# Kernel tuning notes

Measured on AMD Instinct MI355X. Metric: run time of the kernel, lower is better.

The kernel has to match this reference:

```python
import jax, jax.numpy as jnp
import numpy as np

HIDDEN_DIM = 2048
CODE_DIM = 256
CODEBOOK_SIZE = 512
FC_DIMS = [1024, 512]
BATCH = 16384
EPS = 1e-5
NEG_SLOPE = 0.01  # PyTorch LeakyReLU default


def _linear_init(key, fan_in, fan_out):
    # kaiming_uniform_(a=sqrt(3)) ~= U(-1/sqrt(fan_in), 1/sqrt(fan_in)) scaled; use uniform bound
    bound = 1.0 / np.sqrt(fan_in)
    return jax.random.uniform(key, (fan_in, fan_out), jnp.float32, -bound, bound)


def setup_inputs() -> dict:
    key = jax.random.key(0)
    ks = jax.random.split(key, 16)
    h = jax.random.normal(ks[0], (BATCH, HIDDEN_DIM), jnp.float32)
    # encoder: Linear(2048->1024, no bias), BN, LReLU, Linear(1024->512, no bias), BN, LReLU, Linear(512->256, bias)
    enc_w1 = _linear_init(ks[1], HIDDEN_DIM, FC_DIMS[0])
    enc_bn1_g = jnp.ones((FC_DIMS[0],), jnp.float32)
    enc_bn1_b = jnp.zeros((FC_DIMS[0],), jnp.float32)
    enc_w2 = _linear_init(ks[2], FC_DIMS[0], FC_DIMS[1])
    enc_bn2_g = jnp.ones((FC_DIMS[1],), jnp.float32)
    enc_bn2_b = jnp.zeros((FC_DIMS[1],), jnp.float32)
    enc_w3 = _linear_init(ks[3], FC_DIMS[1], CODE_DIM)
    enc_b3 = jax.random.uniform(ks[4], (CODE_DIM,), jnp.float32, -1/np.sqrt(FC_DIMS[1]), 1/np.sqrt(FC_DIMS[1]))
    # codebook: NearestEmbed weight shape (code_dim, codebook_size)
    codebook = jax.random.normal(ks[5], (CODE_DIM, CODEBOOK_SIZE), jnp.float32)
    # decoder: Linear(256->512, no bias), BN, LReLU, Linear(512->1024, no bias), BN, LReLU, Linear(1024->2048, bias)
    dec_w1 = _linear_init(ks[6], CODE_DIM, FC_DIMS[1])
    dec_bn1_g = jnp.ones((FC_DIMS[1],), jnp.float32)
    dec_bn1_b = jnp.zeros((FC_DIMS[1],), jnp.float32)
    dec_w2 = _linear_init(ks[7], FC_DIMS[1], FC_DIMS[0])
    dec_bn2_g = jnp.ones((FC_DIMS[0],), jnp.float32)
    dec_bn2_b = jnp.zeros((FC_DIMS[0],), jnp.float32)
    dec_w3 = _linear_init(ks[8], FC_DIMS[0], HIDDEN_DIM)
    dec_b3 = jax.random.uniform(ks[9], (HIDDEN_DIM,), jnp.float32, -1/np.sqrt(FC_DIMS[0]), 1/np.sqrt(FC_DIMS[0]))
    return dict(h=h, enc_w1=enc_w1, enc_bn1_g=enc_bn1_g, enc_bn1_b=enc_bn1_b,
                enc_w2=enc_w2, enc_bn2_g=enc_bn2_g, enc_bn2_b=enc_bn2_b,
                enc_w3=enc_w3, enc_b3=enc_b3, codebook=codebook,
                dec_w1=dec_w1, dec_bn1_g=dec_bn1_g, dec_bn1_b=dec_bn1_b,
                dec_w2=dec_w2, dec_bn2_g=dec_bn2_g, dec_bn2_b=dec_bn2_b,
                dec_w3=dec_w3, dec_b3=dec_b3)


def _bn(x, g, b):
    # BatchNorm1d, training mode: biased batch variance, eps=1e-5
    mu = jnp.mean(x, axis=0)
    var = jnp.var(x, axis=0)
    return (x - mu) * jax.lax.rsqrt(var + EPS) * g + b


def _lrelu(x):
    return jnp.where(x >= 0, x, NEG_SLOPE * x)


def _quantize(z_e, codebook):
    # nearest codebook entry; codebook is [code_dim, K]
    # dist[b,k] = ||z_e[b] - codebook[:,k]||^2 (expanded, drop constant ||z||^2 for argmin? keep full for clarity)
    d = (jnp.sum(z_e * z_e, axis=1, keepdims=True)
         - 2.0 * (z_e @ codebook)
         + jnp.sum(codebook * codebook, axis=0)[None, :])  # [B, K]
    idx = jnp.argmin(d, axis=1)  # [B]
    z_q = codebook.T[idx]        # [B, code_dim]
    return z_q, idx


def reference(h, enc_w1, enc_bn1_g, enc_bn1_b, enc_w2, enc_bn2_g, enc_bn2_b,
              enc_w3, enc_b3, codebook,
              dec_w1, dec_bn1_g, dec_bn1_b, dec_w2, dec_bn2_g, dec_bn2_b,
              dec_w3, dec_b3):
    # encoder
    x = _lrelu(_bn(h @ enc_w1, enc_bn1_g, enc_bn1_b))
    x = _lrelu(_bn(x @ enc_w2, enc_bn2_g, enc_bn2_b))
    z_e = x @ enc_w3 + enc_b3  # [B, code_dim]
    # nearest-embed quantization with straight-through estimator
    z_q_raw, code_indices = _quantize(z_e, codebook)
    z_q = z_e + jax.lax.stop_gradient(z_q_raw - z_e)
    # decoder
    y = _lrelu(_bn(z_q @ dec_w1, dec_bn1_g, dec_bn1_b))
    y = _lrelu(_bn(y @ dec_w2, dec_bn2_g, dec_bn2_b))
    h_recon = y @ dec_w3 + dec_b3  # [B, hidden_dim]
    return z_e, z_q, h_recon, code_indices
```

## Files before the change

kernel.cpp:

```cpp
#include <hip/hip_runtime.h>
#include <hip/hip_fp16.h>
#include <cstdint>
#include <cstddef>

typedef _Float16 f16;
typedef _Float16 half8 __attribute__((ext_vector_type(8)));
typedef _Float16 half4 __attribute__((ext_vector_type(4)));
typedef float floatx4 __attribute__((ext_vector_type(4)));

static constexpr size_t NB  = 16384;
static constexpr size_t DH  = 2048;
static constexpr size_t F1  = 1024;
static constexpr size_t F2  = 512;
static constexpr size_t CD  = 256;
static constexpr size_t KCB = 512;

static constexpr size_t ZE_OFF  = 0;
static constexpr size_t ZQ_OFF  = NB * CD;
static constexpr size_t HR_OFF  = 2 * NB * CD;
static constexpr size_t IDX_OFF = 2 * NB * CD + NB * DH;

static constexpr size_t O_HH   = 0;
static constexpr size_t O_HL   = O_HH + NB * DH * 2;
static constexpr size_t R1_END = O_HL + NB * DH * 2;

static constexpr size_t R_X1H = 0;
static constexpr size_t R_X1L = NB * F1 * 2;
static constexpr size_t R_X2F = 2 * NB * F1 * 2;
static constexpr size_t R_X2H = R_X2F + NB * F2 * 4;
static constexpr size_t R_X2L = R_X2H + NB * F2 * 2;
static constexpr size_t R_Y1F = 0;
static constexpr size_t R_Y1H = NB * F2 * 4;
static constexpr size_t R_Y2H = 0;

static constexpr size_t O_W1H = R1_END;
static constexpr size_t O_W1L = O_W1H + F1 * DH * 2;
static constexpr size_t O_W2H = O_W1L + F1 * DH * 2;
static constexpr size_t O_W2L = O_W2H + F2 * F1 * 2;
static constexpr size_t O_W3H = O_W2L + F2 * F1 * 2;
static constexpr size_t O_W3L = O_W3H + CD * F2 * 2;
static constexpr size_t O_CBH = O_W3L + CD * F2 * 2;
static constexpr size_t O_CBL = O_CBH + KCB * CD * 2;
static constexpr size_t O_DW1 = O_CBL + KCB * CD * 2;
static constexpr size_t O_DW2 = O_DW1 + F2 * CD * 2;
static constexpr size_t O_DW3 = O_DW2 + F1 * F2 * 2;
static constexpr size_t O_SUM = O_DW3 + DH * F1 * 2;
static constexpr size_t O_SQ  = O_SUM + 4 * 1024 * 8;
static constexpr size_t O_SC  = O_SQ + 4 * 1024 * 8;
static constexpr size_t O_SH  = O_SC + 4 * 1024 * 4;
static constexpr size_t O_CN  = O_SH + 4 * 1024 * 4;
static constexpr size_t R2    = (O_CN + 4096 + 255) & ~(size_t)255;
static constexpr size_t R2_X1F = R2;
static constexpr size_t R2_ZEH = R2;
static constexpr size_t R2_ZEL = R2 + NB * CD * 2;
static constexpr size_t R2_S   = R2 + 2 * NB * CD * 2;
static constexpr size_t R2_ZQH = R2_S + NB * KCB * 4;
static constexpr size_t R2_Y2F = R2;

#define GLLDS(src, dst)                                                          \
    __builtin_amdgcn_global_load_lds(                                            \
        (const __attribute__((address_space(1))) void*)(src),                    \
        (__attribute__((address_space(3))) void*)(dst), 16, 0, 0)

#define VMCNT(n)  asm volatile("s_waitcnt vmcnt(" #n ")" ::: "memory")
#define LGKMCNT0  asm volatile("s_waitcnt lgkmcnt(0)" ::: "memory")

#define WAITC(n) do { switch (n) {                                               \
    case 0: asm volatile("s_waitcnt lgkmcnt(0)" ::: "memory"); break;            \
    case 1: asm volatile("s_waitcnt lgkmcnt(1)" ::: "memory"); break;            \
    case 2: asm volatile("s_waitcnt lgkmcnt(2)" ::: "memory"); break;            \
    case 3: asm volatile("s_waitcnt lgkmcnt(3)" ::: "memory"); break;            \
    case 4: asm volatile("s_waitcnt lgkmcnt(4)" ::: "memory"); break;            \
    case 5: asm volatile("s_waitcnt lgkmcnt(5)" ::: "memory"); break;            \
    case 6: asm volatile("s_waitcnt lgkmcnt(6)" ::: "memory"); break;            \
    default: asm volatile("s_waitcnt lgkmcnt(7)" ::: "memory"); break; }         \
    __builtin_amdgcn_sched_barrier(0); } while (0)

template<int MW, bool BIAS, bool STATS, bool WSPLIT>
__global__ __launch_bounds__(512)
void gemm3_t(const f16* __restrict__ Ah_, const f16* __restrict__ Al_,
             const f16* __restrict__ Bh_, const f16* __restrict__ Bl_,
             float* __restrict__ C, const float* __restrict__ bias,
             double* __restrict__ ssum, double* __restrict__ ssq,
             f16* __restrict__ zeh, f16* __restrict__ zel,
             int M, int N, int K)
{
    constexpr int BM = MW * 32;
    __shared__ f16 lds[2][2][16384];
    const int tid  = threadIdx.x;
    const int lane = tid & 63;
    const int w    = tid >> 6;
    const int wr   = w >> 2, wn = w & 3;
    const int row0 = blockIdx.x * BM;
    const int col0 = blockIdx.y * 256;

    const int rr8 = lane >> 3;
    const int p   = (lane & 7) ^ rr8;
    const int rr  = w * 32 + rr8;
    const int arr = rr & (BM - 1);
    const f16* srcH = (p < 4) ? (Ah_ + (size_t)(row0 + arr) * K + p * 8)
                              : (Bh_ + (size_t)(col0 + rr) * K + (p - 4) * 8);
    const f16* srcL = (p < 4) ? (Al_ + (size_t)(row0 + arr) * K + p * 8)
                              : (Bl_ + (size_t)(col0 + rr) * K + (p - 4) * 8);
    const int dstBase = w * 32 * 64;
    const int KT = K >> 5;

    floatx4 acc[MW][4];
#pragma unroll
    for (int m = 0; m < MW; ++m)
#pragma unroll
        for (int n = 0; n < 4; ++n)
#pragma unroll
            for (int j = 0; j < 4; ++j) acc[m][n][j] = 0.f;

    const int l15 = lane & 15;
    const int sA  = lane >> 4;

    int rdA[MW], rdB[4];
#pragma unroll
    for (int m = 0; m < MW; ++m) {
        const int rA = wr * (MW * 16) + m * 16 + l15;
        rdA[m] = rA * 64 + ((sA ^ (rA & 7)) << 3);
    }
#pragma unroll
    for (int n = 0; n < 4; ++n) {
        const int rB = wn * 64 + n * 16 + l15;
        rdB[n] = rB * 64 + (((4 + sA) ^ (rB & 7)) << 3);
    }

#pragma unroll
    for (int j = 0; j < 4; ++j)
        GLLDS(srcH + (size_t)j * 8 * K, &lds[0][0][dstBase + j * 512]);
#pragma unroll
    for (int j = 0; j < 4; ++j)
        GLLDS(srcL + (size_t)j * 8 * K, &lds[0][1][dstBase + j * 512]);
    VMCNT(4);
    __builtin_amdgcn_s_barrier();

    half8 afh[MW], afl[MW], bfh[4], bfl[4];

    for (int kt = 0; kt < KT; ++kt) {
        const int cur = kt & 1, nxt = cur ^ 1;
        const int koff = (kt + 1 < KT ? kt + 1 : kt) << 5;
        const f16* plH = lds[cur][0];
        const f16* plL = lds[cur][1];

#pragma unroll
        for (int n = 0; n < 4; ++n) bfh[n] = *(const half8*)(plH + rdB[n]);
        afh[0] = *(const half8*)(plH + rdA[0]);
        afh[1] = *(const half8*)(plH + rdA[1]);
#pragma unroll
        for (int j = 0; j < 4; ++j)
            GLLDS(srcH + (size_t)j * 8 * K + koff, &lds[nxt][0][dstBase + j * 512]);
        WAITC(1);
        __builtin_amdgcn_s_setprio(1);
#pragma unroll
        for (int m = 0; m < MW; ++m) {
            if (m + 2 < MW) afh[m + 2] = *(const half8*)(plH + rdA[m + 2]);
#pragma unroll
            for (int n = 0; n < 4; ++n)
                acc[m][n] = __builtin_amdgcn_mfma_f32_16x16x32_f16(afh[m], bfh[n], acc[m][n], 0, 0, 0);
            if (m + 1 < MW) { if (m + 2 < MW) WAITC(1); else WAITC(0); }
        }
        __builtin_amdgcn_s_setprio(0);
        VMCNT(4);
        __builtin_amdgcn_s_barrier();

#pragma unroll
        for (int n = 0; n < 4; ++n) bfl[n] = *(const half8*)(plL + rdB[n]);
        afl[0] = *(const half8*)(plL + rdA[0]);
        afl[1] = *(const half8*)(plL + rdA[1]);
#pragma unroll
        for (int j = 0; j < 4; ++j)
            GLLDS(srcL + (size_t)j * 8 * K + koff, &lds[nxt][1][dstBase + j * 512]);
        WAITC(2);
        __builtin_amdgcn_s_setprio(1);
#pragma unroll
        for (int m = 0; m < MW; ++m) {
            if (m + 2 < MW) afl[m + 2] = *(const half8*)(plL + rdA[m + 2]);
#pragma unroll
            for (int n = 0; n < 4; ++n)
                acc[m][n] = __builtin_amdgcn_mfma_f32_16x16x32_f16(afh[m], bfl[n], acc[m][n], 0, 0, 0);
        }
#pragma unroll
        for (int m = 0; m < MW; ++m) {
            WAITC(MW - 1 - m);
#pragma unroll
            for (int n = 0; n < 4; ++n)
                acc[m][n] = __builtin_amdgcn_mfma_f32_16x16x32_f16(afl[m], bfh[n], acc[m][n], 0, 0, 0);
        }
        __builtin_amdgcn_s_setprio(0);
        VMCNT(4);
        __builtin_amdgcn_s_barrier();
    }
    VMCNT(0);

    const int cb0 = col0 + wn * 64;
    const int rb0 = row0 + wr * (MW * 16) + (lane >> 4) * 4;
#pragma unroll
    for (int n = 0; n < 4; ++n) {
        const int col = cb0 + n * 16 + l15;
        const float bv = BIAS ? bias[col] : 0.f;
        double sd = 0.0, sq = 0.0;
#pragma unroll
        for (int m = 0; m < MW; ++m) {
            const int row = rb0 + m * 16;
#pragma unroll
            for (int j = 0; j < 4; ++j) {
                const float v = acc[m][n][j] + bv;
                const size_t o = (size_t)(row + j) * N + col;
                C[o] = v;
                if (WSPLIT) {
                    const f16 hv = (f16)v;
                    zeh[o] = hv;
                    zel[o] = (f16)(v - (float)hv);
                }
                if (STATS) { sd += (double)v; sq += (double)v * (double)v; }
            }
        }
        if (STATS) {
            sd += __shfl_xor(sd, 16);
            sd += __shfl_xor(sd, 32);
            sq += __shfl_xor(sq, 16);
            sq += __shfl_xor(sq, 32);
            if (lane < 16) {
                atomicAdd(ssum + col, sd);
                atomicAdd(ssq + col, sq);
            }
        }
    }
}

template<int MW, bool BIAS, bool STATS>
__global__ __launch_bounds__(512)
void gemm1_t(const f16* __restrict__ A_, const f16* __restrict__ B_,
             float* __restrict__ C, const float* __restrict__ bias,
             double* __restrict__ ssum, double* __restrict__ ssq,
             int M, int N, int K)
{
    constexpr int BM = MW * 32;
    __shared__ f16 lds[3][16384];
    const int tid  = threadIdx.x;
    const int lane = tid & 63;
    const int w    = tid >> 6;
    const int wr   = w >> 2, wn = w & 3;
    const int row0 = blockIdx.x * BM;
    const int col0 = blockIdx.y * 256;

    const int rr8 = lane >> 3;
    const int p   = (lane & 7) ^ rr8;
    const int rr  = w * 32 + rr8;
    const int arr = rr & (BM - 1);
    const f16* srcH = (p < 4) ? (A_ + (size_t)(row0 + arr) * K + p * 8)
                              : (B_ + (size_t)(col0 + rr) * K + (p - 4) * 8);
    const int dstBase = w * 32 * 64;
    const int KT = K >> 5;

    floatx4 acc[MW][4];
#pragma unroll
    for (int m = 0; m < MW; ++m)
#pragma unroll
        for (int n = 0; n < 4; ++n)
#pragma unroll
            for (int j = 0; j < 4; ++j) acc[m][n][j] = 0.f;

    const int l15 = lane & 15;
    const int sA  = lane >> 4;

    int rdA[MW], rdB[4];
#pragma unroll
    for (int m = 0; m < MW; ++m) {
        const int rA = wr * (MW * 16) + m * 16 + l15;
        rdA[m] = rA * 64 + ((sA ^ (rA & 7)) << 3);
    }
#pragma unroll
    for (int n = 0; n < 4; ++n) {
        const int rB = wn * 64 + n * 16 + l15;
        rdB[n] = rB * 64 + (((4 + sA) ^ (rB & 7)) << 3);
    }

#pragma unroll
    for (int j = 0; j < 4; ++j)
        GLLDS(srcH + (size_t)j * 8 * K, &lds[0][dstBase + j * 512]);
    {
        const int k1 = (KT > 1 ? 1 : 0) << 5;
#pragma unroll
        for (int j = 0; j < 4; ++j)
            GLLDS(srcH + (size_t)j * 8 * K + k1, &lds[1][dstBase + j * 512]);
    }
    VMCNT(4);
    __builtin_amdgcn_s_barrier();

    half8 afh[MW], bfh[4];

    for (int kt = 0; kt < KT; ++kt) {
        const int cur = kt % 3, tgt = (kt + 2) % 3;
        const int koff = (kt + 2 < KT ? kt + 2 : KT - 1) << 5;
        const f16* plH = lds[cur];

#pragma unroll
        for (int n = 0; n < 4; ++n) bfh[n] = *(const half8*)(plH + rdB[n]);
        afh[0] = *(const half8*)(plH + rdA[0]);
        afh[1] = *(const half8*)(plH + rdA[1]);
#pragma unroll
        for (int j = 0; j < 4; ++j)
            GLLDS(srcH + (size_t)j * 8 * K + koff, &lds[tgt][dstBase + j * 512]);
        WAITC(1);
        __builtin_amdgcn_s_setprio(1);
#pragma unroll
        for (int m = 0; m < MW; ++m) {
            if (m + 2 < MW) afh[m + 2] = *(const half8*)(plH + rdA[m + 2]);
#pragma unroll
            for (int n = 0; n < 4; ++n)
                acc[m][n] = __builtin_amdgcn_mfma_f32_16x16x32_f16(afh[m], bfh[n], acc[m][n], 0, 0, 0);
            if (m + 1 < MW) { if (m + 2 < MW) WAITC(1); else WAITC(0); }
        }
        __builtin_amdgcn_s_setprio(0);
        VMCNT(4);
        __builtin_amdgcn_s_barrier();
    }
    VMCNT(0);

    const int cb0 = col0 + wn * 64;
    const int rb0 = row0 + wr * (MW * 16) + (lane >> 4) * 4;
#pragma unroll
    for (int n = 0; n < 4; ++n) {
        const int col = cb0 + n * 16 + l15;
        const float bv = BIAS ? bias[col] : 0.f;
        double sd = 0.0, sq = 0.0;
#pragma unroll
        for (int m = 0; m < MW; ++m) {
            const int row = rb0 + m * 16;
#pragma unroll
            for (int j = 0; j < 4; ++j) {
                const float v = acc[m][n][j] + bv;
                C[(size_t)(row + j) * N + col] = v;
                if (STATS) { sd += (double)v; sq += (double)v * (double)v; }
            }
        }
        if (STATS) {
            sd += __shfl_xor(sd, 16);
            sd += __shfl_xor(sd, 32);
            sq += __shfl_xor(sq, 16);
            sq += __shfl_xor(sq, 32);
            if (lane < 16) {
                atomicAdd(ssum + col, sd);
                atomicAdd(ssq + col, sq);
            }
        }
    }
}

__global__ void split_f32(const float* __restrict__ X, f16* __restrict__ hi,
                          f16* __restrict__ lo, size_t n4)
{
    const size_t stride = (size_t)gridDim.x * blockDim.x;
    for (size_t i = (size_t)blockIdx.x * blockDim.x + threadIdx.x; i < n4; i += stride) {
        const floatx4 x = ((const floatx4*)X)[i];
        half4 h, l;
#pragma unroll
        for (int j = 0; j < 4; ++j) {
            const float v = x[j];
            const f16 hv = (f16)v;
            h[j] = hv;
            l[j] = (f16)(v - (float)hv);
        }
        ((half4*)hi)[i] = h;
        ((half4*)lo)[i] = l;
    }
}

template<bool SPLIT>
__global__ void bn_apply(const float* __restrict__ X, const float* __restrict__ scale,
                         const float* __restrict__ shift, f16* __restrict__ Yhi,
                         f16* __restrict__ Ylo, size_t n4, int Nmask)
{
    const size_t stride = (size_t)gridDim.x * blockDim.x;
    for (size_t i = (size_t)blockIdx.x * blockDim.x + threadIdx.x; i < n4; i += stride) {
        const floatx4 x = ((const floatx4*)X)[i];
        const int col = (int)((i * 4) & (size_t)Nmask);
        half4 h, l;
#pragma unroll
        for (int j = 0; j < 4; ++j) {
            float v = x[j] * scale[col + j] + shift[col + j];
            v = v >= 0.f ? v : 0.01f * v;
            const f16 hv = (f16)v;
            h[j] = hv;
            if (SPLIT) l[j] = (f16)(v - (float)hv);
        }
        ((half4*)Yhi)[i] = h;
        if (SPLIT) ((half4*)Ylo)[i] = l;
    }
}

__global__ void bn_finalize(const double* __restrict__ ssum, const double* __restrict__ ssq,
                            const float* __restrict__ g, const float* __restrict__ b,
                            float* __restrict__ scale, float* __restrict__ shift, int N)
{
    const int j = blockIdx.x * blockDim.x + threadIdx.x;
    if (j < N) {
        const double inv = 1.0 / (double)NB;
        const double mean = ssum[j] * inv;
        const double var  = ssq[j] * inv - mean * mean;
        const double sc   = (double)g[j] / sqrt(var + 1e-5);
        scale[j] = (float)sc;
        shift[j] = (float)((double)b[j] - mean * sc);
    }
}

template<bool SPLIT>
__global__ void transpose_split(const float* __restrict__ W, f16* __restrict__ Thi,
                                f16* __restrict__ Tlo, int K, int N)
{
    __shared__ float tile[32][33];
    const int x = threadIdx.x;
    const int y = threadIdx.y;
    const int nt = blockIdx.x * 32;
    const int kt = blockIdx.y * 32;
#pragma unroll
    for (int i = 0; i < 32; i += 8)
        tile[y + i][x] = W[(size_t)(kt + y + i) * N + nt + x];
    __syncthreads();
#pragma unroll
    for (int i = 0; i < 32; i += 8) {
        const float v = tile[x][y + i];
        const size_t o = (size_t)(nt + y + i) * K + kt + x;
        const f16 hv = (f16)v;
        Thi[o] = hv;
        if (SPLIT) Tlo[o] = (f16)(v - (float)hv);
    }
}

__global__ void cnorm_kernel(const float* __restrict__ cb, float* __restrict__ cn)
{
    const int k = blockIdx.x * blockDim.x + threadIdx.x;
    if (k < (int)KCB) {
        double s = 0.0;
        for (int d = 0; d < (int)CD; ++d) {
            const float v = cb[(size_t)d * KCB + k];
            s += (double)v * v;
        }
        cn[k] = (float)s;
    }
}

__global__ void argmin_gather(const float* __restrict__ S, const float* __restrict__ cn,
                              const float* __restrict__ cb, float* __restrict__ zq,
                              float* __restrict__ idx_out, f16* __restrict__ zqh)
{
    const int lane = threadIdx.x & 63;
    const int row  = blockIdx.x * 4 + (threadIdx.x >> 6);
    const float* Sr = S + (size_t)row * KCB;
    float best = 3.4e38f;
    int bi = 0;
#pragma unroll
    for (int i = 0; i < 8; ++i) {
        const int k = lane + 64 * i;
        const float d = cn[k] - 2.f * Sr[k];
        if (d < best) { best = d; bi = k; }
    }
#pragma unroll
    for (int off = 32; off > 0; off >>= 1) {
        const float ob = __shfl_xor(best, off);
        const int   oi = __shfl_xor(bi, off);
        if (ob < best || (ob == best && oi < bi)) { best = ob; bi = oi; }
    }
    if (lane == 0) idx_out[row] = (float)bi;
#pragma unroll
    for (int i = 0; i < 4; ++i) {
        const int d = lane + 64 * i;
        const float v = cb[(size_t)d * KCB + bi];
        zq[(size_t)row * CD + d]  = v;
        zqh[(size_t)row * CD + d] = (f16)v;
    }
}

extern "C" void kernel_launch(void* const* d_in, const int* in_sizes, int n_in,
                              void* d_out, int out_size, void* d_ws, size_t ws_size,
                              hipStream_t stream)
{
    (void)in_sizes; (void)n_in; (void)out_size; (void)ws_size;
    const float* h   = (const float*)d_in[0];
    const float* ew1 = (const float*)d_in[1];
    const float* bg1 = (const float*)d_in[2];
    const float* bb1 = (const float*)d_in[3];
    const float* ew2 = (const float*)d_in[4];
    const float* bg2 = (const float*)d_in[5];
    const float* bb2 = (const float*)d_in[6];
    const float* ew3 = (const float*)d_in[7];
    const float* eb3 = (const float*)d_in[8];
    const float* cb  = (const float*)d_in[9];
    const float* dw1 = (const float*)d_in[10];
    const float* dg1 = (const float*)d_in[11];
    const float* db1 = (const float*)d_in[12];
    const float* dw2 = (const float*)d_in[13];
    const float* dg2 = (const float*)d_in[14];
    const float* db2 = (const float*)d_in[15];
    const float* dw3 = (const float*)d_in[16];
    const float* db3 = (const float*)d_in[17];

    char* ws = (char*)d_ws;
    float* out = (float*)d_out;

    f16* Hh  = (f16*)(ws + O_HH);
    f16* Hl  = (f16*)(ws + O_HL);
    f16* W1h = (f16*)(ws + O_W1H);
    f16* W1l = (f16*)(ws + O_W1L);
    f16* W2h = (f16*)(ws + O_W2H);
    f16* W2l = (f16*)(ws + O_W2L);
    f16* W3h = (f16*)(ws + O_W3H);
    f16* W3l = (f16*)(ws + O_W3L);
    f16* CBh = (f16*)(ws + O_CBH);
    f16* CBl = (f16*)(ws + O_CBL);
    f16* D1t = (f16*)(ws + O_DW1);
    f16* D2t = (f16*)(ws + O_DW2);
    f16* D3t = (f16*)(ws + O_DW3);
    double* sum0 = (double*)(ws + O_SUM);
    double* sq0  = (double*)(ws + O_SQ);
    float* sc0 = (float*)(ws + O_SC);
    float* sh0 = (float*)(ws + O_SH);
    float* cn  = (float*)(ws + O_CN);

    float* X1f = (float*)(ws + R2_X1F);
    f16*  X1h = (f16*)(ws + R_X1H);
    f16*  X1l = (f16*)(ws + R_X1L);
    float* X2f = (float*)(ws + R_X2F);
    f16*  X2h = (f16*)(ws + R_X2H);
    f16*  X2l = (f16*)(ws + R_X2L);
    f16*  Zeh = (f16*)(ws + R2_ZEH);
    f16*  Zel = (f16*)(ws + R2_ZEL);
    float* Sb  = (float*)(ws + R2_S);
    f16*  Zqh = (f16*)(ws + R2_ZQH);
    float* Y1f = (float*)(ws + R_Y1F);
    f16*  Y1h = (f16*)(ws + R_Y1H);
    float* Y2f = (float*)(ws + R2_Y2F);
    f16*  Y2h = (f16*)(ws + R_Y2H);

    hipMemsetAsync(ws + O_SUM, 0, 4 * 1024 * 8 * 2, stream);

    split_f32<<<2048, 256, 0, stream>>>(h, Hh, Hl, NB * DH / 4);
    transpose_split<true ><<<dim3(F1 / 32, DH / 32), dim3(32, 8), 0, stream>>>(ew1, W1h, W1l, DH, F1);
    transpose_split<true ><<<dim3(F2 / 32, F1 / 32), dim3(32, 8), 0, stream>>>(ew2, W2h, W2l, F1, F2);
    transpose_split<true ><<<dim3(CD / 32, F2 / 32), dim3(32, 8), 0, stream>>>(ew3, W3h, W3l, F2, CD);
    transpose_split<true ><<<dim3(KCB / 32, CD / 32), dim3(32, 8), 0, stream>>>(cb, CBh, CBl, CD, KCB);
    transpose_split<false><<<dim3(F2 / 32, CD / 32), dim3(32, 8), 0, stream>>>(dw1, D1t, nullptr, CD, F2);
    transpose_split<false><<<dim3(F1 / 32, F2 / 32), dim3(32, 8), 0, stream>>>(dw2, D2t, nullptr, F2, F1);
    transpose_split<false><<<dim3(DH / 32, F1 / 32), dim3(32, 8), 0, stream>>>(dw3, D3t, nullptr, F1, DH);

    gemm3_t<8, false, true, false><<<dim3(NB / 256, F1 / 256), 512, 0, stream>>>(
        Hh, Hl, W1h, W1l, X1f, nullptr, sum0, sq0, nullptr, nullptr, NB, F1, DH);
    bn_finalize<<<4, 256, 0, stream>>>(sum0, sq0, bg1, bb1, sc0, sh0, F1);
    bn_apply<true><<<2048, 256, 0, stream>>>(X1f, sc0, sh0, X1h, X1l, NB * F1 / 4, (int)F1 - 1);

    gemm3_t<4, false, true, false><<<dim3(NB / 128, F2 / 256), 512, 0, stream>>>(
        X1h, X1l, W2h, W2l, X2f, nullptr, sum0 + 1024, sq0 + 1024, nullptr, nullptr, NB, F2, F1);
    bn_finalize<<<2, 256, 0, stream>>>(sum0 + 1024, sq0 + 1024, bg2, bb2, sc0 + 1024, sh0 + 1024, F2);
    bn_apply<true><<<2048, 256, 0, stream>>>(X2f, sc0 + 1024, sh0 + 1024, X2h, X2l, NB * F2 / 4, (int)F2 - 1);

    gemm3_t<4, true, false, true><<<dim3(NB / 128, CD / 256), 512, 0, stream>>>(
        X2h, X2l, W3h, W3l, out + ZE_OFF, eb3, nullptr, nullptr, Zeh, Zel, NB, CD, F2);

    cnorm_kernel<<<2, 256, 0, stream>>>(cb, cn);
    gemm3_t<4, false, false, false><<<dim3(NB / 128, KCB / 256), 512, 0, stream>>>(
        Zeh, Zel, CBh, CBl, Sb, nullptr, nullptr, nullptr, nullptr, nullptr, NB, KCB, CD);
    argmin_gather<<<NB / 4, 256, 0, stream>>>(Sb, cn, cb, out + ZQ_OFF, out + IDX_OFF, Zqh);

    gemm1_t<4, false, true><<<dim3(NB / 128, F2 / 256), 512, 0, stream>>>(
        Zqh, D1t, Y1f, nullptr, sum0 + 2048, sq0 + 2048, NB, F2, CD);
    bn_finalize<<<2, 256, 0, stream>>>(sum0 + 2048, sq0 + 2048, dg1, db1, sc0 + 2048, sh0 + 2048, F2);
    bn_apply<false><<<2048, 256, 0, stream>>>(Y1f, sc0 + 2048, sh0 + 2048, Y1h, nullptr, NB * F2 / 4, (int)F2 - 1);

    gemm1_t<8, false, true><<<dim3(NB / 256, F1 / 256), 512, 0, stream>>>(
        Y1h, D2t, Y2f, nullptr, sum0 + 3072, sq0 + 3072, NB, F1, F2);
    bn_finalize<<<4, 256, 0, stream>>>(sum0 + 3072, sq0 + 3072, dg2, db2, sc0 + 3072, sh0 + 3072, F1);
    bn_apply<false><<<2048, 256, 0, stream>>>(Y2f, sc0 + 3072, sh0 + 3072, Y2h, nullptr, NB * F1 / 4, (int)F1 - 1);

    gemm1_t<8, true, false><<<dim3(NB / 256, DH / 256), 512, 0, stream>>>(
        Y2h, D3t, out + HR_OFF, db3, nullptr, nullptr, NB, DH, F1);
}
```

Before: 606.4 us.

## Switch GEMMs to 128x128 tiles with 256-thread blocks and merge weight prep kernels

Every GEMM now uses one 128x128 tile shape with 4 waves per block instead of 256x256 or 128x256 tiles with 8 waves. This quarters or halves the LDS footprint per block and gives more blocks, so more blocks can be resident per CU. The cost is lower operand reuse per tile and more global traffic. The seven weight transpose/split launches and the codebook-norm kernel are also merged into one prep_weights launch to cut launch overhead.

```diff
diff --git a/kernel.cpp b/kernel.cpp
--- a/kernel.cpp
+++ b/kernel.cpp
@@ -63,7 +63,6 @@
         (__attribute__((address_space(3))) void*)(dst), 16, 0, 0)
 
 #define VMCNT(n)  asm volatile("s_waitcnt vmcnt(" #n ")" ::: "memory")
-#define LGKMCNT0  asm volatile("s_waitcnt lgkmcnt(0)" ::: "memory")
 
 #define WAITC(n) do { switch (n) {                                               \
     case 0: asm volatile("s_waitcnt lgkmcnt(0)" ::: "memory"); break;            \
@@ -76,38 +75,36 @@
     default: asm volatile("s_waitcnt lgkmcnt(7)" ::: "memory"); break; }         \
     __builtin_amdgcn_sched_barrier(0); } while (0)
 
-template<int MW, bool BIAS, bool STATS, bool WSPLIT>
-__global__ __launch_bounds__(512)
-void gemm3_t(const f16* __restrict__ Ah_, const f16* __restrict__ Al_,
-             const f16* __restrict__ Bh_, const f16* __restrict__ Bl_,
-             float* __restrict__ C, const float* __restrict__ bias,
-             double* __restrict__ ssum, double* __restrict__ ssq,
-             f16* __restrict__ zeh, f16* __restrict__ zel,
-             int M, int N, int K)
-{
-    constexpr int BM = MW * 32;
-    __shared__ f16 lds[2][2][16384];
+template<bool BIAS, bool STATS, bool WSPLIT>
+__global__ __launch_bounds__(256)
+void g3s(const f16* __restrict__ Ah_, const f16* __restrict__ Al_,
+         const f16* __restrict__ Bh_, const f16* __restrict__ Bl_,
+         float* __restrict__ C, const float* __restrict__ bias,
+         double* __restrict__ ssum, double* __restrict__ ssq,
+         f16* __restrict__ zeh, f16* __restrict__ zel,
+         int M, int N, int K)
+{
+    __shared__ f16 lds[2][2][8192];
     const int tid  = threadIdx.x;
     const int lane = tid & 63;
     const int w    = tid >> 6;
-    const int wr   = w >> 2, wn = w & 3;
-    const int row0 = blockIdx.x * BM;
-    const int col0 = blockIdx.y * 256;
+    const int wr   = w >> 1, wn = w & 1;
+    const int row0 = blockIdx.x * 128;
+    const int col0 = blockIdx.y * 128;
 
     const int rr8 = lane >> 3;
     const int p   = (lane & 7) ^ rr8;
     const int rr  = w * 32 + rr8;
-    const int arr = rr & (BM - 1);
-    const f16* srcH = (p < 4) ? (Ah_ + (size_t)(row0 + arr) * K + p * 8)
+    const f16* srcH = (p < 4) ? (Ah_ + (size_t)(row0 + rr) * K + p * 8)
                               : (Bh_ + (size_t)(col0 + rr) * K + (p - 4) * 8);
-    const f16* srcL = (p < 4) ? (Al_ + (size_t)(row0 + arr) * K + p * 8)
+    const f16* srcL = (p < 4) ? (Al_ + (size_t)(row0 + rr) * K + p * 8)
                               : (Bl_ + (size_t)(col0 + rr) * K + (p - 4) * 8);
     const int dstBase = w * 32 * 64;
     const int KT = K >> 5;
 
-    floatx4 acc[MW][4];
-#pragma unroll
-    for (int m = 0; m < MW; ++m)
+    floatx4 acc[4][4];
+#pragma unroll
+    for (int m = 0; m < 4; ++m)
 #pragma unroll
         for (int n = 0; n < 4; ++n)
 #pragma unroll
@@ -116,10 +113,10 @@
     const int l15 = lane & 15;
     const int sA  = lane >> 4;
 
-    int rdA[MW], rdB[4];
-#pragma unroll
-    for (int m = 0; m < MW; ++m) {
-        const int rA = wr * (MW * 16) + m * 16 + l15;
+    int rdA[4], rdB[4];
+#pragma unroll
+    for (int m = 0; m < 4; ++m) {
+        const int rA = wr * 64 + m * 16 + l15;
         rdA[m] = rA * 64 + ((sA ^ (rA & 7)) << 3);
     }
 #pragma unroll
@@ -137,7 +134,7 @@
     VMCNT(4);
     __builtin_amdgcn_s_barrier();
 
-    half8 afh[MW], afl[MW], bfh[4], bfl[4];
+    half8 afh[4], afl[4], bfh[4], bfl[4];
 
     for (int kt = 0; kt < KT; ++kt) {
         const int cur = kt & 1, nxt = cur ^ 1;
@@ -155,12 +152,12 @@
         WAITC(1);
         __builtin_amdgcn_s_setprio(1);
 #pragma unroll
-        for (int m = 0; m < MW; ++m) {
-            if (m + 2 < MW) afh[m + 2] = *(const half8*)(plH + rdA[m + 2]);
+        for (int m = 0; m < 4; ++m) {
+            if (m + 2 < 4) afh[m + 2] = *(const half8*)(plH + rdA[m + 2]);
 #pragma unroll
             for (int n = 0; n < 4; ++n)
                 acc[m][n] = __builtin_amdgcn_mfma_f32_16x16x32_f16(afh[m], bfh[n], acc[m][n], 0, 0, 0);
-            if (m + 1 < MW) { if (m + 2 < MW) WAITC(1); else WAITC(0); }
+            if (m + 1 < 4) { if (m + 2 < 4) WAITC(1); else WAITC(0); }
         }
         __builtin_amdgcn_s_setprio(0);
         VMCNT(4);
@@ -176,15 +173,15 @@
         WAITC(2);
         __builtin_amdgcn_s_setprio(1);
 #pragma unroll
-        for (int m = 0; m < MW; ++m) {
-            if (m + 2 < MW) afl[m + 2] = *(const half8*)(plL + rdA[m + 2]);
+        for (int m = 0; m < 4; ++m) {
+            if (m + 2 < 4) afl[m + 2] = *(const half8*)(plL + rdA[m + 2]);
 #pragma unroll
             for (int n = 0; n < 4; ++n)
                 acc[m][n] = __builtin_amdgcn_mfma_f32_16x16x32_f16(afh[m], bfl[n], acc[m][n], 0, 0, 0);
         }
 #pragma unroll
-        for (int m = 0; m < MW; ++m) {
-            WAITC(MW - 1 - m);
+        for (int m = 0; m < 4; ++m) {
+            WAITC(3 - m);
 #pragma unroll
             for (int n = 0; n < 4; ++n)
                 acc[m][n] = __builtin_amdgcn_mfma_f32_16x16x32_f16(afl[m], bfh[n], acc[m][n], 0, 0, 0);
@@ -196,14 +193,14 @@
     VMCNT(0);
 
     const int cb0 = col0 + wn * 64;
-    const int rb0 = row0 + wr * (MW * 16) + (lane >> 4) * 4;
+    const int rb0 = row0 + wr * 64 + (lane >> 4) * 4;
 #pragma unroll
     for (int n = 0; n < 4; ++n) {
         const int col = cb0 + n * 16 + l15;
         const float bv = BIAS ? bias[col] : 0.f;
         double sd = 0.0, sq = 0.0;
 #pragma unroll
-        for (int m = 0; m < MW; ++m) {
+        for (int m = 0; m < 4; ++m) {
             const int row = rb0 + m * 16;
 #pragma unroll
             for (int j = 0; j < 4; ++j) {
@@ -231,34 +228,32 @@
     }
 }
 
-template<int MW, bool BIAS, bool STATS>
-__global__ __launch_bounds__(512)
-void gemm1_t(const f16* __restrict__ A_, const f16* __restrict__ B_,
-             float* __restrict__ C, const float* __restrict__ bias,
-             double* __restrict__ ssum, double* __restrict__ ssq,
-             int M, int N, int K)
-{
-    constexpr int BM = MW * 32;
-    __shared__ f16 lds[3][16384];
+template<bool BIAS, bool STATS>
+__global__ __launch_bounds__(256)
+void g1s(const f16* __restrict__ A_, const f16* __restrict__ B_,
+         float* __restrict__ C, const float* __restrict__ bias,
+         double* __restrict__ ssum, double* __restrict__ ssq,
+         int M, int N, int K)
+{
+    __shared__ f16 lds[3][8192];
     const int tid  = threadIdx.x;
     const int lane = tid & 63;
     const int w    = tid >> 6;
-    const int wr   = w >> 2, wn = w & 3;
-    const int row0 = blockIdx.x * BM;
-    const int col0 = blockIdx.y * 256;
+    const int wr   = w >> 1, wn = w & 1;
+    const int row0 = blockIdx.x * 128;
+    const int col0 = blockIdx.y * 128;
 
     const int rr8 = lane >> 3;
     const int p   = (lane & 7) ^ rr8;
     const int rr  = w * 32 + rr8;
-    const int arr = rr & (BM - 1);
-    const f16* srcH = (p < 4) ? (A_ + (size_t)(row0 + arr) * K + p * 8)
+    const f16* srcH = (p < 4) ? (A_ + (size_t)(row0 + rr) * K + p * 8)
                               : (B_ + (size_t)(col0 + rr) * K + (p - 4) * 8);
     const int dstBase = w * 32 * 64;
     const int KT = K >> 5;
 
-    floatx4 acc[MW][4];
-#pragma unroll
-    for (int m = 0; m < MW; ++m)
+    floatx4 acc[4][4];
+#pragma unroll
+    for (int m = 0; m < 4; ++m)
 #pragma unroll
         for (int n = 0; n < 4; ++n)
 #pragma unroll
@@ -267,10 +262,10 @@
     const int l15 = lane & 15;
     const int sA  = lane >> 4;
 
-    int rdA[MW], rdB[4];
-#pragma unroll
-    for (int m = 0; m < MW; ++m) {
-        const int rA = wr * (MW * 16) + m * 16 + l15;
+    int rdA[4], rdB[4];
+#pragma unroll
+    for (int m = 0; m < 4; ++m) {
+        const int rA = wr * 64 + m * 16 + l15;
         rdA[m] = rA * 64 + ((sA ^ (rA & 7)) << 3);
     }
 #pragma unroll
@@ -291,7 +286,7 @@
     VMCNT(4);
     __builtin_amdgcn_s_barrier();
 
-    half8 afh[MW], bfh[4];
+    half8 afh[4], bfh[4];
 
     for (int kt = 0; kt < KT; ++kt) {
         const int cur = kt % 3, tgt = (kt + 2) % 3;
@@ -308,12 +303,12 @@
         WAITC(1);
         __builtin_amdgcn_s_setprio(1);
 #pragma unroll
-        for (int m = 0; m < MW; ++m) {
-            if (m + 2 < MW) afh[m + 2] = *(const half8*)(plH + rdA[m + 2]);
+        for (int m = 0; m < 4; ++m) {
+            if (m + 2 < 4) afh[m + 2] = *(const half8*)(plH + rdA[m + 2]);
 #pragma unroll
             for (int n = 0; n < 4; ++n)
                 acc[m][n] = __builtin_amdgcn_mfma_f32_16x16x32_f16(afh[m], bfh[n], acc[m][n], 0, 0, 0);
-            if (m + 1 < MW) { if (m + 2 < MW) WAITC(1); else WAITC(0); }
+            if (m + 1 < 4) { if (m + 2 < 4) WAITC(1); else WAITC(0); }
         }
         __builtin_amdgcn_s_setprio(0);
         VMCNT(4);
@@ -322,14 +317,14 @@
     VMCNT(0);
 
     const int cb0 = col0 + wn * 64;
-    const int rb0 = row0 + wr * (MW * 16) + (lane >> 4) * 4;
+    const int rb0 = row0 + wr * 64 + (lane >> 4) * 4;
 #pragma unroll
     for (int n = 0; n < 4; ++n) {
         const int col = cb0 + n * 16 + l15;
         const float bv = BIAS ? bias[col] : 0.f;
         double sd = 0.0, sq = 0.0;
 #pragma unroll
-        for (int m = 0; m < MW; ++m) {
+        for (int m = 0; m < 4; ++m) {
             const int row = rb0 + m * 16;
 #pragma unroll
             for (int j = 0; j < 4; ++j) {
@@ -408,15 +403,15 @@
     }
 }
 
-template<bool SPLIT>
-__global__ void transpose_split(const float* __restrict__ W, f16* __restrict__ Thi,
-                                f16* __restrict__ Tlo, int K, int N)
+__device__ __forceinline__ void tr_body(const float* __restrict__ W, f16* __restrict__ Thi,
+                                        f16* __restrict__ Tlo, int K, int N,
+                                        int bx, int by, bool split)
 {
     __shared__ float tile[32][33];
     const int x = threadIdx.x;
     const int y = threadIdx.y;
-    const int nt = blockIdx.x * 32;
-    const int kt = blockIdx.y * 32;
+    const int nt = bx * 32;
+    const int kt = by * 32;
 #pragma unroll
     for (int i = 0; i < 32; i += 8)
         tile[y + i][x] = W[(size_t)(kt + y + i) * N + nt + x];
@@ -427,20 +422,40 @@
         const size_t o = (size_t)(nt + y + i) * K + kt + x;
         const f16 hv = (f16)v;
         Thi[o] = hv;
-        if (SPLIT) Tlo[o] = (f16)(v - (float)hv);
-    }
-}
-
-__global__ void cnorm_kernel(const float* __restrict__ cb, float* __restrict__ cn)
-{
-    const int k = blockIdx.x * blockDim.x + threadIdx.x;
-    if (k < (int)KCB) {
-        double s = 0.0;
-        for (int d = 0; d < (int)CD; ++d) {
-            const float v = cb[(size_t)d * KCB + k];
-            s += (double)v * v;
-        }
-        cn[k] = (float)s;
+        if (split) Tlo[o] = (f16)(v - (float)hv);
+    }
+}
+
+__global__ void prep_weights(const float* __restrict__ ew1, const float* __restrict__ ew2,
+                             const float* __restrict__ ew3, const float* __restrict__ cbk,
+                             const float* __restrict__ dw1, const float* __restrict__ dw2,
+                             const float* __restrict__ dw3,
+                             f16* __restrict__ W1h, f16* __restrict__ W1l,
+                             f16* __restrict__ W2h, f16* __restrict__ W2l,
+                             f16* __restrict__ W3h, f16* __restrict__ W3l,
+                             f16* __restrict__ CBh, f16* __restrict__ CBl,
+                             f16* __restrict__ D1t, f16* __restrict__ D2t,
+                             f16* __restrict__ D3t, float* __restrict__ cn)
+{
+    const int b = blockIdx.x;
+    if (b < 2048)      tr_body(ew1, W1h, W1l, DH, F1, b % 32, b / 32, true);
+    else if (b < 2560) { const int c = b - 2048; tr_body(ew2, W2h, W2l, F1, F2, c % 16, c / 16, true); }
+    else if (b < 2688) { const int c = b - 2560; tr_body(ew3, W3h, W3l, F2, CD, c % 8,  c / 8,  true); }
+    else if (b < 2816) { const int c = b - 2688; tr_body(cbk, CBh, CBl, CD, KCB, c % 16, c / 16, true); }
+    else if (b < 2944) { const int c = b - 2816; tr_body(dw1, D1t, nullptr, CD, F2, c % 16, c / 16, false); }
+    else if (b < 3456) { const int c = b - 2944; tr_body(dw2, D2t, nullptr, F2, F1, c % 32, c / 32, false); }
+    else if (b < 5504) { const int c = b - 3456; tr_body(dw3, D3t, nullptr, F1, DH, c % 64, c / 64, false); }
+    else {
+        const int tid = threadIdx.y * 32 + threadIdx.x;
+        const int k = (b - 5504) * 256 + tid;
+        if (k < (int)KCB) {
+            double s = 0.0;
+            for (int d = 0; d < (int)CD; ++d) {
+                const float v = cbk[(size_t)d * KCB + k];
+                s += (double)v * v;
+            }
+            cn[k] = (float)s;
+        }
     }
 }
 
@@ -539,42 +554,36 @@
     hipMemsetAsync(ws + O_SUM, 0, 4 * 1024 * 8 * 2, stream);
 
     split_f32<<<2048, 256, 0, stream>>>(h, Hh, Hl, NB * DH / 4);
-    transpose_split<true ><<<dim3(F1 / 32, DH / 32), dim3(32, 8), 0, stream>>>(ew1, W1h, W1l, DH, F1);
-    transpose_split<true ><<<dim3(F2 / 32, F1 / 32), dim3(32, 8), 0, stream>>>(ew2, W2h, W2l, F1, F2);
-    transpose_split<true ><<<dim3(CD / 32, F2 / 32), dim3(32, 8), 0, stream>>>(ew3, W3h, W3l, F2, CD);
-    transpose_split<true ><<<dim3(KCB / 32, CD / 32), dim3(32, 8), 0, stream>>>(cb, CBh, CBl, CD, KCB);
-    transpose_split<false><<<dim3(F2 / 32, CD / 32), dim3(32, 8), 0, stream>>>(dw1, D1t, nullptr, CD, F2);
-    transpose_split<false><<<dim3(F1 / 32, F2 / 32), dim3(32, 8), 0, stream>>>(dw2, D2t, nullptr, F2, F1);
-    transpose_split<false><<<dim3(DH / 32, F1 / 32), dim3(32, 8), 0, stream>>>(dw3, D3t, nullptr, F1, DH);
-
-    gemm3_t<8, false, true, false><<<dim3(NB / 256, F1 / 256), 512, 0, stream>>>(
+    prep_weights<<<5506, dim3(32, 8), 0, stream>>>(ew1, ew2, ew3, cb, dw1, dw2, dw3,
+        W1h, W1l, W2h, W2l, W3h, W3l, CBh, CBl, D1t, D2t, D3t, cn);
+
+    g3s<false, true, false><<<dim3(NB / 128, F1 / 128), 256, 0, stream>>>(
         Hh, Hl, W1h, W1l, X1f, nullptr, sum0, sq0, nullptr, nullptr, NB, F1, DH);
     bn_finalize<<<4, 256, 0, stream>>>(sum0, sq0, bg1, bb1, sc0, sh0, F1);
     bn_apply<true><<<2048, 256, 0, stream>>>(X1f, sc0, sh0, X1h, X1l, NB * F1 / 4, (int)F1 - 1);
 
-    gemm3_t<4, false, true, false><<<dim3(NB / 128, F2 / 256), 512, 0, stream>>>(
+    g3s<false, true, false><<<dim3(NB / 128, F2 / 128), 256, 0, stream>>>(
         X1h, X1l, W2h, W2l, X2f, nullptr, sum0 + 1024, sq0 + 1024, nullptr, nullptr, NB, F2, F1);
     bn_finalize<<<2, 256, 0, stream>>>(sum0 + 1024, sq0 + 1024, bg2, bb2, sc0 + 1024, sh0 + 1024, F2);
     bn_apply<true><<<2048, 256, 0, stream>>>(X2f, sc0 + 1024, sh0 + 1024, X2h, X2l, NB * F2 / 4, (int)F2 - 1);
 
-    gemm3_t<4, true, false, true><<<dim3(NB / 128, CD / 256), 512, 0, stream>>>(
+    g3s<true, false, true><<<dim3(NB / 128, CD / 128), 256, 0, stream>>>(
         X2h, X2l, W3h, W3l, out + ZE_OFF, eb3, nullptr, nullptr, Zeh, Zel, NB, CD, F2);
 
-    cnorm_kernel<<<2, 256, 0, stream>>>(cb, cn);
-    gemm3_t<4, false, false, false><<<dim3(NB / 128, KCB / 256), 512, 0, stream>>>(
+    g3s<false, false, false><<<dim3(NB / 128, KCB / 128), 256, 0, stream>>>(
         Zeh, Zel, CBh, CBl, Sb, nullptr, nullptr, nullptr, nullptr, nullptr, NB, KCB, CD);
     argmin_gather<<<NB / 4, 256, 0, stream>>>(Sb, cn, cb, out + ZQ_OFF, out + IDX_OFF, Zqh);
 
-    gemm1_t<4, false, true><<<dim3(NB / 128, F2 / 256), 512, 0, stream>>>(
+    g1s<false, true><<<dim3(NB / 128, F2 / 128), 256, 0, stream>>>(
         Zqh, D1t, Y1f, nullptr, sum0 + 2048, sq0 + 2048, NB, F2, CD);
     bn_finalize<<<2, 256, 0, stream>>>(sum0 + 2048, sq0 + 2048, dg1, db1, sc0 + 2048, sh0 + 2048, F2);
     bn_apply<false><<<2048, 256, 0, stream>>>(Y1f, sc0 + 2048, sh0 + 2048, Y1h, nullptr, NB * F2 / 4, (int)F2 - 1);
 
-    gemm1_t<8, false, true><<<dim3(NB / 256, F1 / 256), 512, 0, stream>>>(
+    g1s<false, true><<<dim3(NB / 128, F1 / 128), 256, 0, stream>>>(
         Y1h, D2t, Y2f, nullptr, sum0 + 3072, sq0 + 3072, NB, F1, F2);
     bn_finalize<<<4, 256, 0, stream>>>(sum0 + 3072, sq0 + 3072, dg2, db2, sc0 + 3072, sh0 + 3072, F1);
     bn_apply<false><<<2048, 256, 0, stream>>>(Y2f, sc0 + 3072, sh0 + 3072, Y2h, nullptr, NB * F1 / 4, (int)F1 - 1);
 
-    gemm1_t<8, true, false><<<dim3(NB / 256, DH / 256), 512, 0, stream>>>(
+    g1s<true, false><<<dim3(NB / 128, DH / 128), 256, 0, stream>>>(
         Y2h, D3t, out + HR_OFF, db3, nullptr, nullptr, NB, DH, F1);
 }
```

Measured after the change: 667.2 us. +10.0%, slower.
